# Kernel optimization log

Measured on AMD Instinct MI355X. Metric: run time of the kernel, lower is better.

Reference implementation:

```python
import jax, jax.numpy as jnp
import numpy as np

DIM, CTX_DIM, HEADS, HIDDEN = 1024, 768, 16, 4096
HEAD_DIM = DIM // HEADS
SCALE = HEAD_DIM ** -0.5


def _layernorm(x, w, b, eps=1e-5):
    mu = jnp.mean(x, axis=-1, keepdims=True)
    var = jnp.var(x, axis=-1, keepdims=True)
    return (x - mu) * jax.lax.rsqrt(var + eps) * w + b


def _heads(t):  # [B, L, H*D] -> [B, H, L, D]
    B, L, _ = t.shape
    return t.reshape(B, L, HEADS, HEAD_DIM).transpose(0, 2, 1, 3)


def _merge(t):  # [B, H, L, D] -> [B, L, H*D]
    B, H, L, D = t.shape
    return t.transpose(0, 2, 1, 3).reshape(B, L, H * D)


def _attn(xq, xkv, qw, qb, kw, kb, vw, vb, pw, pb):
    q = _heads(xq @ qw.T + qb)
    k = _heads(xkv @ kw.T + kb)
    v = _heads(xkv @ vw.T + vb)
    scores = jnp.einsum('bhld,bhsd->bhls', q, k) * SCALE
    probs = jax.nn.softmax(scores, axis=-1)
    out = _merge(jnp.einsum('bhls,bhsd->bhld', probs, v))
    return out @ pw.T + pb


def setup_inputs() -> dict:
    key = jax.random.key(0)
    ks = jax.random.split(key, 16)
    s = 0.02
    d = {
        'x': jax.random.normal(ks[0], (4, 2048, DIM), jnp.float32),
        'context': jax.random.normal(ks[1], (4, 77, CTX_DIM), jnp.float32),
        'ln1_w': jnp.ones((DIM,)), 'ln1_b': jnp.zeros((DIM,)),
        'ln2_w': jnp.ones((DIM,)), 'ln2_b': jnp.zeros((DIM,)),
        'ln3_w': jnp.ones((DIM,)), 'ln3_b': jnp.zeros((DIM,)),
        'sa_qw': jax.random.normal(ks[2], (DIM, DIM)) * s, 'sa_qb': jnp.zeros((DIM,)),
        'sa_kw': jax.random.normal(ks[3], (DIM, DIM)) * s, 'sa_kb': jnp.zeros((DIM,)),
        'sa_vw': jax.random.normal(ks[4], (DIM, DIM)) * s, 'sa_vb': jnp.zeros((DIM,)),
        'sa_pw': jax.random.normal(ks[5], (DIM, DIM)) * s, 'sa_pb': jnp.zeros((DIM,)),
        'ca_qw': jax.random.normal(ks[6], (DIM, DIM)) * s, 'ca_qb': jnp.zeros((DIM,)),
        'ca_kw': jax.random.normal(ks[7], (DIM, CTX_DIM)) * s, 'ca_kb': jnp.zeros((DIM,)),
        'ca_vw': jax.random.normal(ks[8], (DIM, CTX_DIM)) * s, 'ca_vb': jnp.zeros((DIM,)),
        'ca_pw': jax.random.normal(ks[9], (DIM, DIM)) * s, 'ca_pb': jnp.zeros((DIM,)),
        'fc1_w': jax.random.normal(ks[10], (HIDDEN, DIM)) * s, 'fc1_b': jnp.zeros((HIDDEN,)),
        'fc2_w': jax.random.normal(ks[11], (DIM, HIDDEN)) * s, 'fc2_b': jnp.zeros((DIM,)),
    }
    return d


def reference(x, context, ln1_w, ln1_b, ln2_w, ln2_b, ln3_w, ln3_b,
              sa_qw, sa_qb, sa_kw, sa_kb, sa_vw, sa_vb, sa_pw, sa_pb,
              ca_qw, ca_qb, ca_kw, ca_kb, ca_vw, ca_vb, ca_pw, ca_pb,
              fc1_w, fc1_b, fc2_w, fc2_b):
    h = _layernorm(x, ln1_w, ln1_b)
    x = x + _attn(h, h, sa_qw, sa_qb, sa_kw, sa_kb, sa_vw, sa_vb, sa_pw, sa_pb)
    h = _layernorm(x, ln2_w, ln2_b)
    x = x + _attn(h, context, ca_qw, ca_qb, ca_kw, ca_kb, ca_vw, ca_vb, ca_pw, ca_pb)
    h = _layernorm(x, ln3_w, ln3_b)
    h = jax.nn.gelu(h @ fc1_w.T + fc1_b, approximate=False)  # torch nn.GELU = exact
    x = x + (h @ fc2_w.T + fc2_b)
    return x
```

## Files before the change

### kernel.cpp

```cpp
#include <hip/hip_runtime.h>
#include <hip/hip_bf16.h>
#include <cstdint>
#include <cstddef>

typedef __attribute__((ext_vector_type(8))) short bf16x8;
typedef __attribute__((ext_vector_type(4))) float f32x4;
typedef __attribute__((ext_vector_type(16))) float f32x16;

__device__ __forceinline__ unsigned short f2bf(float f) {
  union { float f; unsigned u; } c; c.f = f;
  unsigned r = c.u + 0x7FFFu + ((c.u >> 16) & 1u);
  return (unsigned short)(r >> 16);
}

__device__ __forceinline__ unsigned cvtpk(float lo, float hi) {
  unsigned r;
  asm("v_cvt_pk_bf16_f32 %0, %1, %2" : "=v"(r) : "v"(lo), "v"(hi));
  return r;
}

__device__ __forceinline__ int xcd_swz(int bid, int nwg) {
  const int cpx = nwg >> 3;
  return (bid & 7) * cpx + (bid >> 3);
}

typedef const __attribute__((address_space(1))) unsigned int* gas_ptr;
typedef __attribute__((address_space(3))) unsigned int* las_ptr;

__device__ __forceinline__ void gload16(const unsigned short* g, unsigned short* l) {
  __builtin_amdgcn_global_load_lds((gas_ptr)g, (las_ptr)l, 16, 0, 0);
}

struct WJ { const float* s; unsigned short* d; int nblk; };
struct WJobs { WJ j[10]; };

__global__ void wconv_k(WJobs jb) {
  const int bid = blockIdx.x;
  int base = 0, ji = -1;
  #pragma unroll
  for (int k = 0; k < 10; ++k) {
    const int nb = jb.j[k].nblk;
    if (ji < 0) { if (bid < base + nb) ji = k; else base += nb; }
  }
  const int i = (bid - base) * 256 + threadIdx.x;
  float4 v = ((const float4*)jb.j[ji].s)[i];
  ushort4 o;
  o.x = f2bf(v.x); o.y = f2bf(v.y); o.z = f2bf(v.z); o.w = f2bf(v.w);
  ((ushort4*)jb.j[ji].d)[i] = o;
}

__global__ void ctxpad_k(const float* __restrict__ ctx, unsigned short* __restrict__ out) {
  int i = blockIdx.x * blockDim.x + threadIdx.x;
  if (i >= 512 * 192) return;
  int r = i / 192, c4 = i % 192;
  int b = r >> 7, s = r & 127;
  ushort4 o = {0, 0, 0, 0};
  if (s < 77) {
    float4 v = ((const float4*)(ctx + (size_t)(b * 77 + s) * 768))[c4];
    o.x = f2bf(v.x); o.y = f2bf(v.y); o.z = f2bf(v.z); o.w = f2bf(v.w);
  }
  ((ushort4*)out)[i] = o;
}

__global__ __launch_bounds__(256)
void ln_k(const float* __restrict__ x, const float* __restrict__ w,
          const float* __restrict__ b, unsigned short* __restrict__ out) {
  int row = blockIdx.x, tid = threadIdx.x;
  float4 v = ((const float4*)(x + (size_t)row * 1024))[tid];
  float s = v.x + v.y + v.z + v.w;
  float s2 = v.x * v.x + v.y * v.y + v.z * v.z + v.w * v.w;
  #pragma unroll
  for (int m = 1; m < 64; m <<= 1) { s += __shfl_xor(s, m); s2 += __shfl_xor(s2, m); }
  __shared__ float ps[4], ps2[4];
  int wv = tid >> 6;
  if ((tid & 63) == 0) { ps[wv] = s; ps2[wv] = s2; }
  __syncthreads();
  s = ps[0] + ps[1] + ps[2] + ps[3];
  s2 = ps2[0] + ps2[1] + ps2[2] + ps2[3];
  float mu = s * (1.0f / 1024.0f);
  float var = s2 * (1.0f / 1024.0f) - mu * mu;
  float rstd = rsqrtf(var + 1e-5f);
  float4 wv4 = ((const float4*)w)[tid];
  float4 bv4 = ((const float4*)b)[tid];
  ushort4 o;
  o.x = f2bf((v.x - mu) * rstd * wv4.x + bv4.x);
  o.y = f2bf((v.y - mu) * rstd * wv4.y + bv4.y);
  o.z = f2bf((v.z - mu) * rstd * wv4.z + bv4.z);
  o.w = f2bf((v.w - mu) * rstd * wv4.w + bv4.w);
  ((ushort4*)(out + (size_t)row * 1024))[tid] = o;
}

#define SG_A(BUF, H, TE)                                                       \
  _Pragma("unroll")                                                            \
  for (int j = 0; j < AHL; ++j)                                                \
    __builtin_amdgcn_global_load_lds(                                          \
        (gas_ptr)(gA + (TE) + (size_t)((H) * (BM / 2) + j * 64) * (size_t)K),  \
        (las_ptr)(lds_all + (BUF) * AELEMS +                                   \
                  (((H) * (BM / 2) + j * 64) + w * 8) * 64),                   \
        16, 0, 0);

#define SG_B(BUF, H, TE)                                                       \
  _Pragma("unroll")                                                            \
  for (int j = 0; j < 2; ++j)                                                  \
    __builtin_amdgcn_global_load_lds(                                          \
        (gas_ptr)(gB + (TE) + (size_t)((H) * 128 + j * 64) * (size_t)K),       \
        (las_ptr)(lds_all + 2 * AELEMS + (BUF) * BELEMS +                      \
                  (((H) * 128 + j * 64) + w * 8) * 64),                        \
        16, 0, 0);

#define RD_A(MHh, BUF)                                                         \
  _Pragma("unroll")                                                            \
  for (int i = 0; i < MH; ++i)                                                 \
    _Pragma("unroll")                                                          \
    for (int kc = 0; kc < 2; ++kc)                                             \
      af[i][kc] = *(const bf16x8*)((const char*)lds_all +                      \
                    aoff[(MHh) * MH + i][kc] + (BUF) * ABYTES);

#define RD_B(NHh, BUF)                                                         \
  _Pragma("unroll")                                                            \
  for (int i = 0; i < 2; ++i)                                                  \
    _Pragma("unroll")                                                          \
    for (int kc = 0; kc < 2; ++kc)                                             \
      bfr[(NHh) * 2 + i][kc] = *(const bf16x8*)((const char*)lds_all +         \
                    boff[(NHh) * 2 + i][kc] + (BUF) * BBYTES);

#define QUAD(MHh, NHh)                                                         \
  __builtin_amdgcn_s_setprio(1);                                               \
  _Pragma("unroll")                                                            \
  for (int i = 0; i < MH; ++i)                                                 \
    _Pragma("unroll")                                                          \
    for (int j2 = 0; j2 < 2; ++j2)                                             \
      _Pragma("unroll")                                                        \
      for (int kc = 0; kc < 2; ++kc) {                                         \
        const int mi = (MHh) * MH + i, ni = (NHh) * 2 + j2;                    \
        if constexpr (SWAP)                                                    \
          acc[mi][ni] = __builtin_amdgcn_mfma_f32_16x16x32_bf16(               \
              bfr[ni][kc], af[i][kc], acc[mi][ni], 0, 0, 0);                   \
        else                                                                   \
          acc[mi][ni] = __builtin_amdgcn_mfma_f32_16x16x32_bf16(               \
              af[i][kc], bfr[ni][kc], acc[mi][ni], 0, 0, 0);                   \
      }                                                                        \
  __builtin_amdgcn_s_setprio(0);

#define VM_TILE()                                                              \
  if constexpr (BM == 256) asm volatile("s_waitcnt vmcnt(6)" ::: "memory");    \
  else                     asm volatile("s_waitcnt vmcnt(4)" ::: "memory");

#define TILE(BUF, TE)                                                          \
  {                                                                            \
    const int t = t2 + ((TE) / 64);                                            \
                       \
    RD_A(0, BUF) RD_B(0, BUF)                                                  \
    if (t + 1 < NT) { SG_B((BUF) ^ 1, 1, (TE) + 64) }                          \
    __builtin_amdgcn_s_barrier();                                              \
    asm volatile("s_waitcnt lgkmcnt(0)" ::: "memory");                         \
    __builtin_amdgcn_sched_barrier(0);                                         \
    QUAD(0, 0)                                                                 \
    __builtin_amdgcn_s_barrier();                                              \
                    \
    RD_B(1, BUF)                                                               \
    if (t + 2 < NT) { SG_A(BUF, 0, (TE) + 128) }                               \
    __builtin_amdgcn_s_barrier();                                              \
    asm volatile("s_waitcnt lgkmcnt(0)" ::: "memory");                         \
    __builtin_amdgcn_sched_barrier(0);                                         \
    QUAD(0, 1)                                                                 \
    __builtin_amdgcn_s_barrier();                                              \
                    \
    RD_A(1, BUF)                                                               \
    if (t + 2 < NT) { SG_B(BUF, 0, (TE) + 128) }                               \
    __builtin_amdgcn_s_barrier();                                              \
    asm volatile("s_waitcnt lgkmcnt(0)" ::: "memory");                         \
    __builtin_amdgcn_sched_barrier(0);                                         \
    QUAD(1, 0)                                                                 \
    __builtin_amdgcn_s_barrier();                                              \
     \
    if (t + 2 < NT) { SG_A(BUF, 1, (TE) + 128) }                               \
    __builtin_amdgcn_s_barrier();                                              \
    __builtin_amdgcn_sched_barrier(0);                                         \
    QUAD(1, 1)                                                                 \
    if (t + 2 < NT) { VM_TILE() }                                              \
    else            { asm volatile("s_waitcnt vmcnt(0)" ::: "memory"); }       \
    __builtin_amdgcn_s_barrier();                                              \
  }

template<int BM, int EPI, int SWAP>
__global__ __launch_bounds__(512, 2)
void gemm8(const unsigned short* __restrict__ A, const unsigned short* __restrict__ Bw,
           const float* __restrict__ bias0, const float* __restrict__ bias1,
           const float* __restrict__ res, void* __restrict__ C0, void* __restrict__ C1,
           int M, int N, int K, float scale0, int nsplit, int vtL) {
  (void)M;
  constexpr int MI = BM / 32;
  constexpr int MH = MI / 2;
  constexpr int AHL = BM / 128;
  constexpr int AELEMS = BM * 64;
  constexpr int BELEMS = 256 * 64;
  constexpr int ABYTES = AELEMS * 2;
  constexpr int BBYTES = BELEMS * 2;
  __shared__ unsigned short lds_all[2 * AELEMS + 2 * BELEMS];

  const int tid = threadIdx.x;
  const int w = tid >> 6, lane = tid & 63;
  const int wr = w >> 2, wcc = w & 3;
  const int ln = lane & 15, lg = lane >> 4;
  const int nbn = N >> 8;
  const int bid = xcd_swz(blockIdx.x, gridDim.x);
  const int bm = bid / nbn, bn = bid % nbn;
  const int NT = K >> 6;

  const int crow = tid >> 3;
  const int cslot = (tid & 7) ^ (crow & 7);

  const unsigned short* gA = A + ((size_t)(bm * BM) + crow) * K + cslot * 8;
  const unsigned short* gB = Bw + ((size_t)(bn * 256) + crow) * K + cslot * 8;

  int aoff[MI][2], boff[4][2];
  #pragma unroll
  for (int mi = 0; mi < MI; ++mi) {
    const int r = mi * 32 + wr * 16 + ln;
    #pragma unroll
    for (int kc = 0; kc < 2; ++kc)
      aoff[mi][kc] = r * 128 + (((kc * 4 + lg) ^ (r & 7)) * 16);
  }
  #pragma unroll
  for (int ni = 0; ni < 4; ++ni) {
    const int r = ni * 64 + wcc * 16 + ln;
    #pragma unroll
    for (int kc = 0; kc < 2; ++kc)
      boff[ni][kc] = 2 * ABYTES + r * 128 + (((kc * 4 + lg) ^ (r & 7)) * 16);
  }

  bf16x8 af[MH][2], bfr[4][2];
  f32x4 acc[MI][4] = {};

  SG_A(0, 0, 0) SG_B(0, 0, 0) SG_B(0, 1, 0) SG_A(0, 1, 0)
  if (NT > 1) { SG_A(1, 0, 64) SG_B(1, 0, 64) SG_A(1, 1, 64) }
  VM_TILE()
  __builtin_amdgcn_s_barrier();

  for (int t2 = 0; t2 < NT; t2 += 2) {
    TILE(0, 0)
    TILE(1, 64)
    gA += 128; gB += 128;
  }

  const int rowbase = bm * BM + wr * 16;
  const int colbase = bn * 256 + wcc * 16;
  if constexpr (EPI == 1) {
    #pragma unroll
    for (int ni = 0; ni < 4; ++ni) {
      const int col = colbase + ni * 64 + ln;
      const float bv = bias0[col];
      const int hh = col >> 6, dd = col & 63;
      #pragma unroll
      for (int mi = 0; mi < MI; ++mi) {
        const int row0 = rowbase + mi * 32 + lg * 4;
        const int bb = row0 / vtL, ss = row0 % vtL;
        ushort4 pk;
        pk.x = f2bf(acc[mi][ni][0] + bv);
        pk.y = f2bf(acc[mi][ni][1] + bv);
        pk.z = f2bf(acc[mi][ni][2] + bv);
        pk.w = f2bf(acc[mi][ni][3] + bv);
        *(ushort4*)((unsigned short*)C0 + ((size_t)((bb * 16 + hh) * 64 + dd)) * vtL + ss) = pk;
      }
    }
  } else {
    #pragma unroll
    for (int ni = 0; ni < 4; ++ni) {
      const int n0 = colbase + ni * 64 + lg * 4;
      const bool lo = (n0 < nsplit);
      const float* bp = lo ? bias0 : bias1;
      const float sc = lo ? scale0 : 1.0f;
      const int nc = lo ? n0 : n0 - nsplit;
      const int ldc = lo ? nsplit : N - nsplit;
      void* Cp = lo ? C0 : C1;
      const float4 b4 = *(const float4*)(bp + nc);
      #pragma unroll
      for (int mi = 0; mi < MI; ++mi) {
        const size_t mrow = (size_t)rowbase + mi * 32 + ln;
        float v0 = acc[mi][ni][0] + b4.x;
        float v1 = acc[mi][ni][1] + b4.y;
        float v2 = acc[mi][ni][2] + b4.z;
        float v3 = acc[mi][ni][3] + b4.w;
        if constexpr (EPI == 0) {
          ushort4 pk;
          pk.x = f2bf(v0 * sc); pk.y = f2bf(v1 * sc);
          pk.z = f2bf(v2 * sc); pk.w = f2bf(v3 * sc);
          *(ushort4*)((unsigned short*)Cp + mrow * ldc + nc) = pk;
        } else if constexpr (EPI == 2) {
          const float4 r4 = *(const float4*)(res + mrow * ldc + nc);
          float4 o4 = { v0 + r4.x, v1 + r4.y, v2 + r4.z, v3 + r4.w };
          *(float4*)((float*)Cp + mrow * ldc + nc) = o4;
        } else {
          v0 = 0.5f * v0 * (1.0f + erff(v0 * 0.70710678118654752f));
          v1 = 0.5f * v1 * (1.0f + erff(v1 * 0.70710678118654752f));
          v2 = 0.5f * v2 * (1.0f + erff(v2 * 0.70710678118654752f));
          v3 = 0.5f * v3 * (1.0f + erff(v3 * 0.70710678118654752f));
          ushort4 pk;
          pk.x = f2bf(v0); pk.y = f2bf(v1); pk.z = f2bf(v2); pk.w = f2bf(v3);
          *(ushort4*)((unsigned short*)Cp + mrow * ldc + nc) = pk;
        }
      }
    }
  }
}

__global__ __launch_bounds__(256, 4)
void flash_k(const unsigned short* __restrict__ Q, const unsigned short* __restrict__ Kg,
             const unsigned short* __restrict__ VT, unsigned short* __restrict__ O,
             int Lq, int Lkpad, int kvlen) {
  const int qblocks = Lq >> 7;
  const int bid = xcd_swz(blockIdx.x, gridDim.x);
  const int bh = bid / qblocks, qb = bid - bh * qblocks;
  const int b = bh >> 4, h = bh & 15;
  const int tid = threadIdx.x, w = tid >> 6, lane = tid & 63;
  const int l31 = lane & 31, hi = lane >> 5;

  __shared__ unsigned short Ks[2][64 * 64];
  __shared__ unsigned short Vs[2][64 * 64];

  const size_t qrow = (size_t)b * Lq + qb * 128 + w * 32 + l31;
  bf16x8 qf[4];
  #pragma unroll
  for (int ds = 0; ds < 4; ++ds)
    qf[ds] = *(const bf16x8*)(Q + qrow * 1024 + h * 64 + ds * 16 + hi * 8);

  f32x16 oacc[2] = {};
  f32x4 lacc = {};

  const int nst = (kvlen + 63) >> 6;
  const int srow = lane >> 3;
  const int gslot = (lane & 7) ^ srow;

  auto STAGE = [&](int buf, int st) {
    #pragma unroll
    for (int i = 0; i < 2; ++i) {
      const int r = i * 32 + w * 8 + srow;
      gload16(Kg + ((size_t)b * Lkpad + st * 64 + r) * 1024 + h * 64 + gslot * 8,
              &Ks[buf][(i * 32 + w * 8) * 64]);
      gload16(VT + ((size_t)bh * 64 + r) * Lkpad + (size_t)st * 64 + gslot * 8,
              &Vs[buf][(i * 32 + w * 8) * 64]);
    }
  };

  STAGE(0, 0);

  for (int st = 0; st < nst; ++st) {
    const int cur = st & 1;
    __syncthreads();
    if (st + 1 < nst) STAGE(cur ^ 1, st + 1);

    const char* Kb = (const char*)Ks[cur];
    const char* Vb = (const char*)Vs[cur];

    #pragma unroll
    for (int kb = 0; kb < 2; ++kb) {
      f32x16 s = {};
      {
        const int r = kb * 32 + l31;
        const int sw = (r & 7) << 4;
        __builtin_amdgcn_s_setprio(1);
        #pragma unroll
        for (int ds = 0; ds < 4; ++ds) {
          bf16x8 kf = *(const bf16x8*)(Kb + r * 128 + ((ds * 32 + hi * 16) ^ sw));
          s = __builtin_amdgcn_mfma_f32_32x32x16_bf16(kf, qf[ds], s, 0, 0, 0);
        }
        __builtin_amdgcn_s_setprio(0);
      }

      if (st * 64 + 64 > kvlen) {
        const int kbase = st * 64 + kb * 32 + hi * 4;
        #pragma unroll
        for (int r = 0; r < 16; ++r)
          if (kbase + (r & 3) + 8 * (r >> 2) >= kvlen) s[r] = -1e30f;
      }

      #pragma unroll
      for (int r = 0; r < 16; ++r) s[r] = __builtin_amdgcn_exp2f(s[r]);
      #pragma unroll
      for (int rq = 0; rq < 4; ++rq) {
        f32x4 t = { s[rq * 4 + 0], s[rq * 4 + 1], s[rq * 4 + 2], s[rq * 4 + 3] };
        lacc += t;
      }

      bf16x8 pf[2];
      #pragma unroll
      for (int m = 0; m < 2; ++m) {
        unsigned u0 = cvtpk(s[8 * m + 0], s[8 * m + 1]);
        unsigned u1 = cvtpk(s[8 * m + 2], s[8 * m + 3]);
        unsigned u2 = cvtpk(s[8 * m + 4], s[8 * m + 5]);
        unsigned u3 = cvtpk(s[8 * m + 6], s[8 * m + 7]);
        asm volatile("v_permlane32_swap_b32 %0, %1" : "+v"(u0), "+v"(u2));
        asm volatile("v_permlane32_swap_b32 %0, %1" : "+v"(u1), "+v"(u3));
        union { unsigned u[4]; bf16x8 v; } fr;
        fr.u[0] = u0; fr.u[1] = u1; fr.u[2] = u2; fr.u[3] = u3;
        pf[m] = fr.v;
      }

      {
        const int sw2 = (l31 & 7) << 4;
        __builtin_amdgcn_s_setprio(1);
        #pragma unroll
        for (int db = 0; db < 2; ++db) {
          const int r = db * 32 + l31;
          #pragma unroll
          for (int m = 0; m < 2; ++m) {
            bf16x8 vf = *(const bf16x8*)(Vb + r * 128 +
                          ((kb * 64 + m * 32 + hi * 16) ^ sw2));
            oacc[db] = __builtin_amdgcn_mfma_f32_32x32x16_bf16(vf, pf[m], oacc[db], 0, 0, 0);
          }
        }
        __builtin_amdgcn_s_setprio(0);
      }
    }
  }

  float lt = lacc[0] + lacc[1] + lacc[2] + lacc[3];
  lt += __shfl_xor(lt, 32);
  const float inv = 1.0f / lt;
  #pragma unroll
  for (int db = 0; db < 2; ++db)
    #pragma unroll
    for (int rg = 0; rg < 4; ++rg) {
      ushort4 pk;
      pk.x = f2bf(oacc[db][rg * 4 + 0] * inv);
      pk.y = f2bf(oacc[db][rg * 4 + 1] * inv);
      pk.z = f2bf(oacc[db][rg * 4 + 2] * inv);
      pk.w = f2bf(oacc[db][rg * 4 + 3] * inv);
      *(ushort4*)(O + qrow * 1024 + h * 64 + db * 32 + rg * 8 + hi * 4) = pk;
    }
}

extern "C" void kernel_launch(void* const* d_in, const int* in_sizes, int n_in,
                              void* d_out, int out_size, void* d_ws, size_t ws_size,
                              hipStream_t stream) {
  (void)in_sizes; (void)n_in; (void)out_size; (void)ws_size;
  const float* x     = (const float*)d_in[0];
  const float* ctx   = (const float*)d_in[1];
  const float* ln1_w = (const float*)d_in[2];
  const float* ln1_b = (const float*)d_in[3];
  const float* ln2_w = (const float*)d_in[4];
  const float* ln2_b = (const float*)d_in[5];
  const float* ln3_w = (const float*)d_in[6];
  const float* ln3_b = (const float*)d_in[7];
  const float* sa_qw = (const float*)d_in[8];  const float* sa_qb = (const float*)d_in[9];
  const float* sa_kw = (const float*)d_in[10]; const float* sa_kb = (const float*)d_in[11];
  const float* sa_vw = (const float*)d_in[12]; const float* sa_vb = (const float*)d_in[13];
  const float* sa_pw = (const float*)d_in[14]; const float* sa_pb = (const float*)d_in[15];
  const float* ca_qw = (const float*)d_in[16]; const float* ca_qb = (const float*)d_in[17];
  const float* ca_kw = (const float*)d_in[18]; const float* ca_kb = (const float*)d_in[19];
  const float* ca_vw = (const float*)d_in[20]; const float* ca_vb = (const float*)d_in[21];
  const float* ca_pw = (const float*)d_in[22]; const float* ca_pb = (const float*)d_in[23];
  const float* fc1_w = (const float*)d_in[24]; const float* fc1_b = (const float*)d_in[25];
  const float* fc2_w = (const float*)d_in[26]; const float* fc2_b = (const float*)d_in[27];

  char* ws = (char*)d_ws;
  size_t o = 0;
  auto give = [&](size_t bytes) { size_t r = o; o += (bytes + 255) & ~(size_t)255; return r; };
  const size_t SQ = 1048576, SC = 786432, SF = 4194304;
  unsigned short* w_qk  = (unsigned short*)(ws + give(2 * SQ * 2));
  unsigned short* w_v   = (unsigned short*)(ws + give(SQ * 2));
  unsigned short* w_p   = (unsigned short*)(ws + give(SQ * 2));
  unsigned short* w_caq = (unsigned short*)(ws + give(SQ * 2));
  unsigned short* w_cak = (unsigned short*)(ws + give(SC * 2));
  unsigned short* w_cav = (unsigned short*)(ws + give(SC * 2));
  unsigned short* w_cap = (unsigned short*)(ws + give(SQ * 2));
  unsigned short* w_f1  = (unsigned short*)(ws + give(SF * 2));
  unsigned short* w_f2  = (unsigned short*)(ws + give(SF * 2));
  unsigned short* ctxb  = (unsigned short*)(ws + give(512 * 768 * 2));
  unsigned short* hbuf  = (unsigned short*)(ws + give(8192 * 1024 * 2));
  unsigned short* qbuf  = (unsigned short*)(ws + give(8192 * 1024 * 2));
  unsigned short* kbuf  = (unsigned short*)(ws + give(8192 * 1024 * 2));
  unsigned short* vtbuf = (unsigned short*)(ws + give(8192 * 1024 * 2));
  unsigned short* obuf  = (unsigned short*)(ws + give(8192 * 1024 * 2));
  float*          xc    = (float*)(ws + give(8192 * 1024 * 4));
  unsigned short* gbuf  = qbuf;

  const float QSCALE = 0.125f * 1.44269504088896341f;

  WJobs jb;
  jb.j[0] = { sa_qw, w_qk,      (int)(SQ / 1024) };
  jb.j[1] = { sa_kw, w_qk + SQ, (int)(SQ / 1024) };
  jb.j[2] = { sa_vw, w_v,       (int)(SQ / 1024) };
  jb.j[3] = { sa_pw, w_p,       (int)(SQ / 1024) };
  jb.j[4] = { ca_qw, w_caq,     (int)(SQ / 1024) };
  jb.j[5] = { ca_kw, w_cak,     (int)(SC / 1024) };
  jb.j[6] = { ca_vw, w_cav,     (int)(SC / 1024) };
  jb.j[7] = { ca_pw, w_cap,     (int)(SQ / 1024) };
  jb.j[8] = { fc1_w, w_f1,      (int)(SF / 1024) };
  jb.j[9] = { fc2_w, w_f2,      (int)(SF / 1024) };
  int totblk = 0;
  for (int k = 0; k < 10; ++k) totblk += jb.j[k].nblk;

  wconv_k<<<totblk, 256, 0, stream>>>(jb);
  ctxpad_k<<<384, 256, 0, stream>>>(ctx, ctxb);

  ln_k<<<8192, 256, 0, stream>>>(x, ln1_w, ln1_b, hbuf);
  gemm8<256, 0, 1><<<256, 512, 0, stream>>>(hbuf, w_qk, sa_qb, sa_kb, nullptr, qbuf, kbuf,
                                            8192, 2048, 1024, QSCALE, 1024, 0);
  gemm8<128, 1, 0><<<256, 512, 0, stream>>>(hbuf, w_v, sa_vb, nullptr, nullptr, vtbuf, nullptr,
                                            8192, 1024, 1024, 1.0f, 1024, 2048);
  flash_k<<<1024, 256, 0, stream>>>(qbuf, kbuf, vtbuf, obuf, 2048, 2048, 2048);
  gemm8<128, 2, 1><<<256, 512, 0, stream>>>(obuf, w_p, sa_pb, nullptr, x, xc, nullptr,
                                            8192, 1024, 1024, 1.0f, 1024, 0);

  ln_k<<<8192, 256, 0, stream>>>(xc, ln2_w, ln2_b, hbuf);
  gemm8<128, 0, 1><<<256, 512, 0, stream>>>(hbuf, w_caq, ca_qb, nullptr, nullptr, qbuf, nullptr,
                                            8192, 1024, 1024, QSCALE, 1024, 0);
  gemm8<128, 0, 1><<<16, 512, 0, stream>>>(ctxb, w_cak, ca_kb, nullptr, nullptr, kbuf, nullptr,
                                           512, 1024, 768, 1.0f, 1024, 0);
  gemm8<128, 1, 0><<<16, 512, 0, stream>>>(ctxb, w_cav, ca_vb, nullptr, nullptr, vtbuf, nullptr,
                                           512, 1024, 768, 1.0f, 1024, 128);
  flash_k<<<1024, 256, 0, stream>>>(qbuf, kbuf, vtbuf, obuf, 2048, 128, 77);
  gemm8<128, 2, 1><<<256, 512, 0, stream>>>(obuf, w_cap, ca_pb, nullptr, xc, xc, nullptr,
                                            8192, 1024, 1024, 1.0f, 1024, 0);

  ln_k<<<8192, 256, 0, stream>>>(xc, ln3_w, ln3_b, hbuf);
  gemm8<256, 3, 1><<<512, 512, 0, stream>>>(hbuf, w_f1, fc1_b, nullptr, nullptr, gbuf, nullptr,
                                            8192, 4096, 1024, 1.0f, 4096, 0);
  gemm8<128, 2, 1><<<256, 512, 0, stream>>>(gbuf, w_f2, fc2_b, nullptr, xc, d_out, nullptr,
                                            8192, 1024, 4096, 1.0f, 1024, 0);
}
```

Measured before the change: 491.7 us.

## Replace 8-wave GEMM with 4-wave kernel holding larger per-wave tiles

Rewrites the GEMM from 512 threads (8 waves, 2 blocks per CU) to 256 threads (4 waves, 1 block per CU). Each wave now owns an 8xNI accumulator tile. The M tile is fixed at 256 and the N tile becomes the template parameter. All A and B fragments for a K-step are read from LDS up front, with partial lgkmcnt waits, instead of half-tile reloads between MFMA quads. This aims to raise MFMA work per LDS read and cut barrier overhead, at the cost of much higher register pressure and less latency hiding from fewer waves.

```diff
diff --git a/kernel.cpp b/kernel.cpp
--- a/kernel.cpp
+++ b/kernel.cpp
@@ -92,118 +92,124 @@
 
 #define SG_A(BUF, H, TE)                                                       \
   _Pragma("unroll")                                                            \
-  for (int j = 0; j < AHL; ++j)                                                \
+  for (int j = 0; j < 4; ++j)                                                  \
     __builtin_amdgcn_global_load_lds(                                          \
-        (gas_ptr)(gA + (TE) + (size_t)((H) * (BM / 2) + j * 64) * (size_t)K),  \
-        (las_ptr)(lds_all + (BUF) * AELEMS +                                   \
-                  (((H) * (BM / 2) + j * 64) + w * 8) * 64),                   \
+        (gas_ptr)(gA + (TE) + (size_t)((H) * 128 + j * 32) * (size_t)K),       \
+        (las_ptr)(lds_all + (BUF) * AELEMS + (((H) * 128 + j * 32) + w * 8) * 64), \
         16, 0, 0);
 
 #define SG_B(BUF, H, TE)                                                       \
   _Pragma("unroll")                                                            \
-  for (int j = 0; j < 2; ++j)                                                  \
+  for (int j = 0; j < BH; ++j)                                                 \
     __builtin_amdgcn_global_load_lds(                                          \
-        (gas_ptr)(gB + (TE) + (size_t)((H) * 128 + j * 64) * (size_t)K),       \
+        (gas_ptr)(gB + (TE) + (size_t)((H) * (BN / 2) + j * 32) * (size_t)K),  \
         (las_ptr)(lds_all + 2 * AELEMS + (BUF) * BELEMS +                      \
-                  (((H) * 128 + j * 64) + w * 8) * 64),                        \
+                  (((H) * (BN / 2) + j * 32) + w * 8) * 64),                   \
         16, 0, 0);
 
-#define RD_A(MHh, BUF)                                                         \
+#define RD_A(I0, I1, BUF)                                                      \
   _Pragma("unroll")                                                            \
-  for (int i = 0; i < MH; ++i)                                                 \
+  for (int i = (I0); i < (I1); ++i) {                                          \
+    const int r = i * 32 + wr * 16 + ln;                                       \
     _Pragma("unroll")                                                          \
     for (int kc = 0; kc < 2; ++kc)                                             \
-      af[i][kc] = *(const bf16x8*)((const char*)lds_all +                      \
-                    aoff[(MHh) * MH + i][kc] + (BUF) * ABYTES);
-
-#define RD_B(NHh, BUF)                                                         \
+      af[i][kc] = *(const bf16x8*)((const char*)lds_all + (BUF) * ABYTES +     \
+                    r * 128 + (((kc * 4 + lg) ^ (r & 7)) * 16));               \
+  }
+
+#define RD_B(N0, N1, BUF)                                                      \
   _Pragma("unroll")                                                            \
-  for (int i = 0; i < 2; ++i)                                                  \
+  for (int i = (N0); i < (N1); ++i) {                                          \
+    const int r = i * 32 + wcc * 16 + ln;                                      \
     _Pragma("unroll")                                                          \
     for (int kc = 0; kc < 2; ++kc)                                             \
-      bfr[(NHh) * 2 + i][kc] = *(const bf16x8*)((const char*)lds_all +         \
-                    boff[(NHh) * 2 + i][kc] + (BUF) * BBYTES);
+      bfr[i][kc] = *(const bf16x8*)((const char*)lds_all + 2 * ABYTES +        \
+                    (BUF) * BBYTES + r * 128 + (((kc * 4 + lg) ^ (r & 7)) * 16)); \
+  }
 
 #define QUAD(MHh, NHh)                                                         \
   __builtin_amdgcn_s_setprio(1);                                               \
   _Pragma("unroll")                                                            \
-  for (int i = 0; i < MH; ++i)                                                 \
+  for (int i = 0; i < 4; ++i)                                                  \
     _Pragma("unroll")                                                          \
-    for (int j2 = 0; j2 < 2; ++j2)                                             \
+    for (int j2 = 0; j2 < NIH; ++j2)                                           \
       _Pragma("unroll")                                                        \
       for (int kc = 0; kc < 2; ++kc) {                                         \
-        const int mi = (MHh) * MH + i, ni = (NHh) * 2 + j2;                    \
+        const int mi = (MHh) * 4 + i, ni = (NHh) * NIH + j2;                   \
         if constexpr (SWAP)                                                    \
           acc[mi][ni] = __builtin_amdgcn_mfma_f32_16x16x32_bf16(               \
-              bfr[ni][kc], af[i][kc], acc[mi][ni], 0, 0, 0);                   \
+              bfr[ni][kc], af[mi][kc], acc[mi][ni], 0, 0, 0);                  \
         else                                                                   \
           acc[mi][ni] = __builtin_amdgcn_mfma_f32_16x16x32_bf16(               \
-              af[i][kc], bfr[ni][kc], acc[mi][ni], 0, 0, 0);                   \
+              af[mi][kc], bfr[ni][kc], acc[mi][ni], 0, 0, 0);                  \
       }                                                                        \
   __builtin_amdgcn_s_setprio(0);
 
+#define LGK_G1()                                                               \
+  do { if constexpr (BN == 256) asm volatile("s_waitcnt lgkmcnt(15)" ::: "memory"); \
+       else                     asm volatile("s_waitcnt lgkmcnt(12)" ::: "memory"); } while (0)
+
 #define VM_TILE()                                                              \
-  if constexpr (BM == 256) asm volatile("s_waitcnt vmcnt(6)" ::: "memory");    \
-  else                     asm volatile("s_waitcnt vmcnt(4)" ::: "memory");
+  do { if constexpr (BN == 256) asm volatile("s_waitcnt vmcnt(12)" ::: "memory"); \
+       else                     asm volatile("s_waitcnt vmcnt(10)" ::: "memory"); } while (0)
 
 #define TILE(BUF, TE)                                                          \
   {                                                                            \
     const int t = t2 + ((TE) / 64);                                            \
-                       \
-    RD_A(0, BUF) RD_B(0, BUF)                                                  \
+                  \
+    RD_A(0, 4, BUF) RD_B(0, NIH, BUF)                                          \
+    __builtin_amdgcn_sched_barrier(0);                                         \
+    RD_B(NIH, NI, BUF) RD_A(4, 8, BUF)                                         \
     if (t + 1 < NT) { SG_B((BUF) ^ 1, 1, (TE) + 64) }                          \
     __builtin_amdgcn_s_barrier();                                              \
-    asm volatile("s_waitcnt lgkmcnt(0)" ::: "memory");                         \
+    LGK_G1();                                                                  \
     __builtin_amdgcn_sched_barrier(0);                                         \
     QUAD(0, 0)                                                                 \
     __builtin_amdgcn_s_barrier();                                              \
-                    \
-    RD_B(1, BUF)                                                               \
+                                  \
     if (t + 2 < NT) { SG_A(BUF, 0, (TE) + 128) }                               \
     __builtin_amdgcn_s_barrier();                                              \
     asm volatile("s_waitcnt lgkmcnt(0)" ::: "memory");                         \
     __builtin_amdgcn_sched_barrier(0);                                         \
     QUAD(0, 1)                                                                 \
     __builtin_amdgcn_s_barrier();                                              \
-                    \
-    RD_A(1, BUF)                                                               \
+                                                        \
     if (t + 2 < NT) { SG_B(BUF, 0, (TE) + 128) }                               \
     __builtin_amdgcn_s_barrier();                                              \
-    asm volatile("s_waitcnt lgkmcnt(0)" ::: "memory");                         \
     __builtin_amdgcn_sched_barrier(0);                                         \
     QUAD(1, 0)                                                                 \
     __builtin_amdgcn_s_barrier();                                              \
-     \
+              \
     if (t + 2 < NT) { SG_A(BUF, 1, (TE) + 128) }                               \
     __builtin_amdgcn_s_barrier();                                              \
     __builtin_amdgcn_sched_barrier(0);                                         \
     QUAD(1, 1)                                                                 \
-    if (t + 2 < NT) { VM_TILE() }                                              \
+    if (t + 2 < NT) { VM_TILE(); }                                             \
     else            { asm volatile("s_waitcnt vmcnt(0)" ::: "memory"); }       \
     __builtin_amdgcn_s_barrier();                                              \
   }
 
-template<int BM, int EPI, int SWAP>
-__global__ __launch_bounds__(512, 2)
-void gemm8(const unsigned short* __restrict__ A, const unsigned short* __restrict__ Bw,
+template<int BN, int EPI, int SWAP>
+__global__ __launch_bounds__(256, 1)
+void gemm4(const unsigned short* __restrict__ A, const unsigned short* __restrict__ Bw,
            const float* __restrict__ bias0, const float* __restrict__ bias1,
            const float* __restrict__ res, void* __restrict__ C0, void* __restrict__ C1,
            int M, int N, int K, float scale0, int nsplit, int vtL) {
   (void)M;
-  constexpr int MI = BM / 32;
-  constexpr int MH = MI / 2;
-  constexpr int AHL = BM / 128;
-  constexpr int AELEMS = BM * 64;
-  constexpr int BELEMS = 256 * 64;
+  constexpr int NI = BN / 32;
+  constexpr int NIH = NI / 2;
+  constexpr int BH = BN / 64;
+  constexpr int AELEMS = 256 * 64;
+  constexpr int BELEMS = BN * 64;
   constexpr int ABYTES = AELEMS * 2;
   constexpr int BBYTES = BELEMS * 2;
   __shared__ unsigned short lds_all[2 * AELEMS + 2 * BELEMS];
 
   const int tid = threadIdx.x;
   const int w = tid >> 6, lane = tid & 63;
-  const int wr = w >> 2, wcc = w & 3;
+  const int wr = w >> 1, wcc = w & 1;
   const int ln = lane & 15, lg = lane >> 4;
-  const int nbn = N >> 8;
+  const int nbn = N / BN;
   const int bid = xcd_swz(blockIdx.x, gridDim.x);
   const int bm = bid / nbn, bn = bid % nbn;
   const int NT = K >> 6;
@@ -211,31 +217,15 @@
   const int crow = tid >> 3;
   const int cslot = (tid & 7) ^ (crow & 7);
 
-  const unsigned short* gA = A + ((size_t)(bm * BM) + crow) * K + cslot * 8;
-  const unsigned short* gB = Bw + ((size_t)(bn * 256) + crow) * K + cslot * 8;
-
-  int aoff[MI][2], boff[4][2];
-  #pragma unroll
-  for (int mi = 0; mi < MI; ++mi) {
-    const int r = mi * 32 + wr * 16 + ln;
-    #pragma unroll
-    for (int kc = 0; kc < 2; ++kc)
-      aoff[mi][kc] = r * 128 + (((kc * 4 + lg) ^ (r & 7)) * 16);
-  }
-  #pragma unroll
-  for (int ni = 0; ni < 4; ++ni) {
-    const int r = ni * 64 + wcc * 16 + ln;
-    #pragma unroll
-    for (int kc = 0; kc < 2; ++kc)
-      boff[ni][kc] = 2 * ABYTES + r * 128 + (((kc * 4 + lg) ^ (r & 7)) * 16);
-  }
-
-  bf16x8 af[MH][2], bfr[4][2];
-  f32x4 acc[MI][4] = {};
+  const unsigned short* gA = A + ((size_t)(bm * 256) + crow) * K + cslot * 8;
+  const unsigned short* gB = Bw + ((size_t)(bn * BN) + crow) * K + cslot * 8;
+
+  bf16x8 af[8][2], bfr[NI][2];
+  f32x4 acc[8][NI] = {};
 
   SG_A(0, 0, 0) SG_B(0, 0, 0) SG_B(0, 1, 0) SG_A(0, 1, 0)
   if (NT > 1) { SG_A(1, 0, 64) SG_B(1, 0, 64) SG_A(1, 1, 64) }
-  VM_TILE()
+  VM_TILE();
   __builtin_amdgcn_s_barrier();
 
   for (int t2 = 0; t2 < NT; t2 += 2) {
@@ -244,17 +234,17 @@
     gA += 128; gB += 128;
   }
 
-  const int rowbase = bm * BM + wr * 16;
-  const int colbase = bn * 256 + wcc * 16;
+  const int rowb = bm * 256 + wr * 16;
+  const int colb = bn * BN + wcc * 16;
   if constexpr (EPI == 1) {
     #pragma unroll
-    for (int ni = 0; ni < 4; ++ni) {
-      const int col = colbase + ni * 64 + ln;
+    for (int ni = 0; ni < NI; ++ni) {
+      const int col = colb + ni * 32 + ln;
       const float bv = bias0[col];
       const int hh = col >> 6, dd = col & 63;
       #pragma unroll
-      for (int mi = 0; mi < MI; ++mi) {
-        const int row0 = rowbase + mi * 32 + lg * 4;
+      for (int mi = 0; mi < 8; ++mi) {
+        const int row0 = rowb + mi * 32 + lg * 4;
         const int bb = row0 / vtL, ss = row0 % vtL;
         ushort4 pk;
         pk.x = f2bf(acc[mi][ni][0] + bv);
@@ -266,8 +256,8 @@
     }
   } else {
     #pragma unroll
-    for (int ni = 0; ni < 4; ++ni) {
-      const int n0 = colbase + ni * 64 + lg * 4;
+    for (int ni = 0; ni < NI; ++ni) {
+      const int n0 = colb + ni * 32 + lg * 4;
       const bool lo = (n0 < nsplit);
       const float* bp = lo ? bias0 : bias1;
       const float sc = lo ? scale0 : 1.0f;
@@ -276,8 +266,8 @@
       void* Cp = lo ? C0 : C1;
       const float4 b4 = *(const float4*)(bp + nc);
       #pragma unroll
-      for (int mi = 0; mi < MI; ++mi) {
-        const size_t mrow = (size_t)rowbase + mi * 32 + ln;
+      for (int mi = 0; mi < 8; ++mi) {
+        const size_t mrow = (size_t)rowb + mi * 32 + ln;
         float v0 = acc[mi][ni][0] + b4.x;
         float v1 = acc[mi][ni][1] + b4.y;
         float v2 = acc[mi][ni][2] + b4.z;
@@ -496,28 +486,28 @@
   ctxpad_k<<<384, 256, 0, stream>>>(ctx, ctxb);
 
   ln_k<<<8192, 256, 0, stream>>>(x, ln1_w, ln1_b, hbuf);
-  gemm8<256, 0, 1><<<256, 512, 0, stream>>>(hbuf, w_qk, sa_qb, sa_kb, nullptr, qbuf, kbuf,
+  gemm4<256, 0, 1><<<256, 256, 0, stream>>>(hbuf, w_qk, sa_qb, sa_kb, nullptr, qbuf, kbuf,
                                             8192, 2048, 1024, QSCALE, 1024, 0);
-  gemm8<128, 1, 0><<<256, 512, 0, stream>>>(hbuf, w_v, sa_vb, nullptr, nullptr, vtbuf, nullptr,
+  gemm4<128, 1, 0><<<256, 256, 0, stream>>>(hbuf, w_v, sa_vb, nullptr, nullptr, vtbuf, nullptr,
                                             8192, 1024, 1024, 1.0f, 1024, 2048);
   flash_k<<<1024, 256, 0, stream>>>(qbuf, kbuf, vtbuf, obuf, 2048, 2048, 2048);
-  gemm8<128, 2, 1><<<256, 512, 0, stream>>>(obuf, w_p, sa_pb, nullptr, x, xc, nullptr,
+  gemm4<128, 2, 1><<<256, 256, 0, stream>>>(obuf, w_p, sa_pb, nullptr, x, xc, nullptr,
                                             8192, 1024, 1024, 1.0f, 1024, 0);
 
   ln_k<<<8192, 256, 0, stream>>>(xc, ln2_w, ln2_b, hbuf);
-  gemm8<128, 0, 1><<<256, 512, 0, stream>>>(hbuf, w_caq, ca_qb, nullptr, nullptr, qbuf, nullptr,
+  gemm4<128, 0, 1><<<256, 256, 0, stream>>>(hbuf, w_caq, ca_qb, nullptr, nullptr, qbuf, nullptr,
                                             8192, 1024, 1024, QSCALE, 1024, 0);
-  gemm8<128, 0, 1><<<16, 512, 0, stream>>>(ctxb, w_cak, ca_kb, nullptr, nullptr, kbuf, nullptr,
+  gemm4<128, 0, 1><<<16, 256, 0, stream>>>(ctxb, w_cak, ca_kb, nullptr, nullptr, kbuf, nullptr,
                                            512, 1024, 768, 1.0f, 1024, 0);
-  gemm8<128, 1, 0><<<16, 512, 0, stream>>>(ctxb, w_cav, ca_vb, nullptr, nullptr, vtbuf, nullptr,
+  gemm4<128, 1, 0><<<16, 256, 0, stream>>>(ctxb, w_cav, ca_vb, nullptr, nullptr, vtbuf, nullptr,
                                            512, 1024, 768, 1.0f, 1024, 128);
   flash_k<<<1024, 256, 0, stream>>>(qbuf, kbuf, vtbuf, obuf, 2048, 128, 77);
-  gemm8<128, 2, 1><<<256, 512, 0, stream>>>(obuf, w_cap, ca_pb, nullptr, xc, xc, nullptr,
+  gemm4<128, 2, 1><<<256, 256, 0, stream>>>(obuf, w_cap, ca_pb, nullptr, xc, xc, nullptr,
                                             8192, 1024, 1024, 1.0f, 1024, 0);
 
   ln_k<<<8192, 256, 0, stream>>>(xc, ln3_w, ln3_b, hbuf);
-  gemm8<256, 3, 1><<<512, 512, 0, stream>>>(hbuf, w_f1, fc1_b, nullptr, nullptr, gbuf, nullptr,
+  gemm4<256, 3, 1><<<512, 256, 0, stream>>>(hbuf, w_f1, fc1_b, nullptr, nullptr, gbuf, nullptr,
                                             8192, 4096, 1024, 1.0f, 4096, 0);
-  gemm8<128, 2, 1><<<256, 512, 0, stream>>>(gbuf, w_f2, fc2_b, nullptr, xc, d_out, nullptr,
+  gemm4<128, 2, 1><<<256, 256, 0, stream>>>(gbuf, w_f2, fc2_b, nullptr, xc, d_out, nullptr,
                                             8192, 1024, 4096, 1.0f, 1024, 0);
 }
```

New measurement: 595.8 us. 1.21x slower.
